# Kernel optimization log

Measured on AMD Instinct MI355X. Metric: run time of the kernel, lower is better.

The kernel has to match this reference:

```python
import jax, jax.numpy as jnp
import numpy as np

N_NODES = 100000
N_EDGES = 1600000
F_IN = 512
HEADS = 8
C1 = 8            # hidden per head in conv1
N_CLASSES = 40
NEG_SLOPE = 0.2
EPS = 1e-16


def setup_inputs() -> dict:
    key = jax.random.key(0)
    ks = jax.random.split(key, 12)
    x = jax.random.normal(ks[0], (N_NODES, F_IN), dtype=jnp.float32)
    # edges with src != dst (PyG SuperGAT removes then re-adds self-loops)
    src = jax.random.randint(ks[1], (N_EDGES,), 0, N_NODES)
    off = jax.random.randint(ks[2], (N_EDGES,), 1, N_NODES)
    dst = (src + off) % N_NODES
    edge_index = jnp.stack([src, dst]).astype(jnp.int64)
    def glorot(k, shape):
        fan = shape[0] + shape[-1]
        return jax.random.uniform(k, shape, jnp.float32, -1.0, 1.0) * np.sqrt(6.0 / fan)
    W1 = glorot(ks[3], (F_IN, HEADS * C1))
    att_l1 = glorot(ks[4], (HEADS, C1))
    att_r1 = glorot(ks[5], (HEADS, C1))
    b1 = jnp.zeros((HEADS * C1,), jnp.float32)
    W2 = glorot(ks[6], (HEADS * C1, HEADS * N_CLASSES))
    att_l2 = glorot(ks[7], (HEADS, N_CLASSES))
    att_r2 = glorot(ks[8], (HEADS, N_CLASSES))
    b2 = jnp.zeros((N_CLASSES,), jnp.float32)
    return {"x": x, "edge_index": edge_index, "W1": W1, "att_l1": att_l1,
            "att_r1": att_r1, "b1": b1, "W2": W2, "att_l2": att_l2,
            "att_r2": att_r2, "b2": b2}


def supergat_conv(x, edge_index, W, att_l, att_r, bias, concat):
    """SuperGATConv with attention_type='MX', eval mode (no dropout)."""
    N = x.shape[0]
    H, C = att_l.shape
    xw = (x @ W).reshape(N, H, C)
    loops = jnp.arange(N)
    src = jnp.concatenate([edge_index[0], loops])  # j (source)
    dst = jnp.concatenate([edge_index[1], loops])  # i (target)
    x_j = xw[src]                                   # [E,H,C]
    x_i = xw[dst]                                   # [E,H,C]
    # MX attention: GO score gated by sigmoid of DP logits
    logits = jnp.einsum('ehc,ehc->eh', x_i, x_j)
    alpha = jnp.einsum('ehc,hc->eh', x_j, att_l) + jnp.einsum('ehc,hc->eh', x_i, att_r)
    alpha = alpha * jax.nn.sigmoid(logits)
    alpha = jax.nn.leaky_relu(alpha, NEG_SLOPE)
    # segment softmax over incoming edges of each destination node
    amax = jax.ops.segment_max(alpha, dst, num_segments=N)
    e = jnp.exp(alpha - amax[dst])
    denom = jax.ops.segment_sum(e, dst, num_segments=N)
    a = e / (denom[dst] + EPS)
    out = jax.ops.segment_sum(x_j * a[..., None], dst, num_segments=N)  # [N,H,C]
    out = out.reshape(N, H * C) if concat else out.mean(axis=1)
    return out + bias


def reference(x, edge_index, W1, att_l1, att_r1, b1, W2, att_l2, att_r2, b2):
    # eval mode: F.dropout(p=0.6) is identity, att_loss is 0
    h = jax.nn.elu(supergat_conv(x, edge_index, W1, att_l1, att_r1, b1, concat=True))
    out = supergat_conv(h, edge_index, W2, att_l2, att_r2, b2, concat=False)
    att_loss = jnp.float32(0.0)
    return jax.nn.log_softmax(out, axis=-1), att_loss
```

## Files before the change

kernel.cpp:

```cpp
#include <hip/hip_runtime.h>
#include <cstdint>

#define N_NODES 100000
#define N_EDGES 1600000
#define SCAN_NB 196

typedef short bf16x8 __attribute__((ext_vector_type(8)));
typedef float f32x4 __attribute__((ext_vector_type(4)));
typedef float f32x2 __attribute__((ext_vector_type(2)));

__device__ __forceinline__ uint16_t f2bf(float f) {
    uint32_t b = __float_as_uint(f);
    return (uint16_t)((b + 0x7fffu + ((b >> 16) & 1u)) >> 16);
}
__device__ __forceinline__ float bfval(uint16_t u) {
    return __uint_as_float(((uint32_t)u) << 16);
}
__device__ __forceinline__ float blo(uint32_t u) { return __uint_as_float(u << 16); }
__device__ __forceinline__ float bhi(uint32_t u) { return __uint_as_float(u & 0xffff0000u); }

__global__ void cvt_w1(const float* __restrict__ W1, uint16_t* __restrict__ whi,
                       uint16_t* __restrict__ wlo) {
    int gid = blockIdx.x * 256 + threadIdx.x;
    int c = gid & 63, kg = gid >> 6;
    uint32_t dh[4], dl[4];
    #pragma unroll
    for (int t = 0; t < 4; ++t) {
        float v0 = W1[(kg * 8 + 2 * t) * 64 + c];
        float v1 = W1[(kg * 8 + 2 * t + 1) * 64 + c];
        uint16_t h0 = f2bf(v0), h1 = f2bf(v1);
        uint16_t l0 = f2bf(v0 - bfval(h0)), l1 = f2bf(v1 - bfval(h1));
        dh[t] = h0 | ((uint32_t)h1 << 16);
        dl[t] = l0 | ((uint32_t)l1 << 16);
    }
    *(uint4*)(whi + (long)c * 512 + kg * 8) = make_uint4(dh[0], dh[1], dh[2], dh[3]);
    *(uint4*)(wlo + (long)c * 512 + kg * 8) = make_uint4(dl[0], dl[1], dl[2], dl[3]);
}

__global__ void cvt_w2(const float* __restrict__ W2, uint16_t* __restrict__ w2T) {
    int c = blockIdx.x * 64 + threadIdx.x;
    if (c >= 320) return;
    for (int kg = 0; kg < 8; ++kg) {
        uint32_t d[4];
        #pragma unroll
        for (int t = 0; t < 4; ++t) {
            float v0 = W2[(kg * 8 + 2 * t) * 320 + c];
            float v1 = W2[(kg * 8 + 2 * t + 1) * 320 + c];
            d[t] = f2bf(v0) | ((uint32_t)f2bf(v1) << 16);
        }
        *(uint4*)(w2T + (long)c * 64 + kg * 8) = make_uint4(d[0], d[1], d[2], d[3]);
    }
}

__global__ __launch_bounds__(256) void wvec_k(const float* __restrict__ W2,
        const float* __restrict__ attl, const float* __restrict__ attr,
        float* __restrict__ wl2, float* __restrict__ wr2) {
    int t = blockIdx.x * 256 + threadIdx.x;
    if (t >= 512) return;
    int h = t >> 6, k = t & 63;
    float sl = 0.f, sr = 0.f;
    #pragma unroll 8
    for (int c = 0; c < 40; ++c) {
        float w = W2[k * 320 + h * 40 + c];
        sl += w * attl[h * 40 + c];
        sr += w * attr[h * 40 + c];
    }
    wl2[t] = sl; wr2[t] = sr;
}

__global__ __launch_bounds__(512) void gemm1_mfma(const float* __restrict__ x,
        const uint16_t* __restrict__ w1hi, const uint16_t* __restrict__ w1lo,
        float* __restrict__ xw1) {
    __shared__ __align__(16) char Ah[128 * 144];
    __shared__ __align__(16) char Al[128 * 144];
    __shared__ __align__(16) char Bh[64 * 144];
    __shared__ __align__(16) char Bl[64 * 144];
    int tid = threadIdx.x;
    int l = tid & 63, w = tid >> 6;
    long base = (long)blockIdx.x * 128;
    f32x4 acc[4];
    #pragma unroll
    for (int ct = 0; ct < 4; ++ct)
        #pragma unroll
        for (int j = 0; j < 4; ++j) acc[ct][j] = 0.f;

    for (int kb = 0; kb < 512; kb += 64) {
        __syncthreads();
        #pragma unroll
        for (int it = 0; it < 2; ++it) {
            int idx = tid + it * 512;
            int row = idx >> 3, kc = idx & 7;
            long r = base + row; if (r >= N_NODES) r = N_NODES - 1;
            const float4* p = (const float4*)(x + r * 512 + kb + kc * 8);
            float4 f0 = p[0], f1 = p[1];
            float v[8] = {f0.x, f0.y, f0.z, f0.w, f1.x, f1.y, f1.z, f1.w};
            uint32_t dh[4], dl[4];
            #pragma unroll
            for (int t = 0; t < 4; ++t) {
                uint16_t h0 = f2bf(v[2 * t]),     h1 = f2bf(v[2 * t + 1]);
                uint16_t l0 = f2bf(v[2 * t] - bfval(h0));
                uint16_t l1 = f2bf(v[2 * t + 1] - bfval(h1));
                dh[t] = h0 | ((uint32_t)h1 << 16);
                dl[t] = l0 | ((uint32_t)l1 << 16);
            }
            *(uint4*)(Ah + row * 144 + kc * 16) = make_uint4(dh[0], dh[1], dh[2], dh[3]);
            *(uint4*)(Al + row * 144 + kc * 16) = make_uint4(dl[0], dl[1], dl[2], dl[3]);
        }
        {
            int c = tid >> 3, kc = tid & 7;
            *(uint4*)(Bh + c * 144 + kc * 16) =
                *(const uint4*)(w1hi + (long)c * 512 + kb + kc * 8);
            *(uint4*)(Bl + c * 144 + kc * 16) =
                *(const uint4*)(w1lo + (long)c * 512 + kb + kc * 8);
        }
        __syncthreads();
        #pragma unroll
        for (int kk = 0; kk < 2; ++kk) {
            int aoff = (w * 16 + (l & 15)) * 144 + kk * 64 + (l >> 4) * 16;
            bf16x8 ah = *(const bf16x8*)(Ah + aoff);
            bf16x8 alo = *(const bf16x8*)(Al + aoff);
            #pragma unroll
            for (int ct = 0; ct < 4; ++ct) {
                int boff = (ct * 16 + (l & 15)) * 144 + kk * 64 + (l >> 4) * 16;
                bf16x8 bh = *(const bf16x8*)(Bh + boff);
                bf16x8 bl = *(const bf16x8*)(Bl + boff);
                acc[ct] = __builtin_amdgcn_mfma_f32_16x16x32_bf16(ah, bh, acc[ct], 0, 0, 0);
                acc[ct] = __builtin_amdgcn_mfma_f32_16x16x32_bf16(alo, bh, acc[ct], 0, 0, 0);
                acc[ct] = __builtin_amdgcn_mfma_f32_16x16x32_bf16(ah, bl, acc[ct], 0, 0, 0);
            }
        }
    }
    int nrow = w * 16 + (l >> 4) * 4;
    #pragma unroll
    for (int ct = 0; ct < 4; ++ct)
        #pragma unroll
        for (int j = 0; j < 4; ++j) {
            long node = base + nrow + j;
            if (node < N_NODES) xw1[node * 64 + ct * 16 + (l & 15)] = acc[ct][j];
        }
}

__global__ __launch_bounds__(512) void gemm2_mfma(const float* __restrict__ h,
        const uint16_t* __restrict__ w2T, uint16_t* __restrict__ xw2) {
    __shared__ __align__(16) char Bsm[320 * 144];
    int tid = threadIdx.x;
    int l = tid & 63, w = tid >> 6;
    long base = (long)blockIdx.x * 128;
    #pragma unroll
    for (int it = 0; it < 5; ++it) {
        int idx = tid + it * 512;
        int c = idx >> 3, kc = idx & 7;
        *(uint4*)(Bsm + c * 144 + kc * 16) = *(const uint4*)(w2T + (long)c * 64 + kc * 8);
    }
    long n0 = base + w * 16 + (l & 15);
    long nld = n0 < N_NODES ? n0 : N_NODES - 1;
    bf16x8 ah[2], alo[2];
    #pragma unroll
    for (int kk = 0; kk < 2; ++kk) {
        const float4* p = (const float4*)(h + nld * 64 + kk * 32 + (l >> 4) * 8);
        float4 f0 = p[0], f1 = p[1];
        float v[8] = {f0.x, f0.y, f0.z, f0.w, f1.x, f1.y, f1.z, f1.w};
        bf16x8 hv, lv;
        #pragma unroll
        for (int t = 0; t < 8; ++t) {
            uint16_t hh = f2bf(v[t]);
            hv[t] = (short)hh;
            lv[t] = (short)f2bf(v[t] - bfval(hh));
        }
        ah[kk] = hv; alo[kk] = lv;
    }
    __syncthreads();
    f32x4 acc[20];
    #pragma unroll
    for (int ct = 0; ct < 20; ++ct)
        #pragma unroll
        for (int j = 0; j < 4; ++j) acc[ct][j] = 0.f;
    #pragma unroll
    for (int ct = 0; ct < 20; ++ct) {
        #pragma unroll
        for (int kk = 0; kk < 2; ++kk) {
            bf16x8 b = *(const bf16x8*)(Bsm + (ct * 16 + (l & 15)) * 144 + kk * 64 + (l >> 4) * 16);
            acc[ct] = __builtin_amdgcn_mfma_f32_16x16x32_bf16(b, ah[kk], acc[ct], 0, 0, 0);
            acc[ct] = __builtin_amdgcn_mfma_f32_16x16x32_bf16(b, alo[kk], acc[ct], 0, 0, 0);
        }
    }
    if (n0 < N_NODES) {
        #pragma unroll
        for (int ct = 0; ct < 20; ++ct) {
            uint32_t d0 = f2bf(acc[ct][0]) | ((uint32_t)f2bf(acc[ct][1]) << 16);
            uint32_t d1 = f2bf(acc[ct][2]) | ((uint32_t)f2bf(acc[ct][3]) << 16);
            int cb = ct * 16 + (l >> 4) * 4;
            *(uint32_t*)(xw2 + n0 * 320 + cb) = d0;
            *(uint32_t*)(xw2 + n0 * 320 + cb + 2) = d1;
        }
    }
}

__global__ void hist_k(const int* __restrict__ dst, int* __restrict__ deg) {
    int e = blockIdx.x * blockDim.x + threadIdx.x;
    if (e < N_EDGES) atomicAdd(&deg[dst[e]], 1);
}

__global__ __launch_bounds__(512) void scan_a(const int* __restrict__ deg,
        int* __restrict__ offs, int* __restrict__ btot) {
    __shared__ int sh[512];
    int t = threadIdx.x;
    int g = blockIdx.x * 512 + t;
    int v = (g < N_NODES) ? deg[g] : 0;
    sh[t] = v;
    __syncthreads();
    #pragma unroll
    for (int o = 1; o < 512; o <<= 1) {
        int add = (t >= o) ? sh[t - o] : 0;
        __syncthreads();
        sh[t] += add;
        __syncthreads();
    }
    if (g < N_NODES) offs[g] = sh[t] - v;
    if (t == 511) btot[blockIdx.x] = sh[511];
}

__global__ __launch_bounds__(256) void scan_b(int* __restrict__ btot) {
    __shared__ int sh[256];
    int t = threadIdx.x;
    int v = (t < SCAN_NB) ? btot[t] : 0;
    sh[t] = v;
    __syncthreads();
    #pragma unroll
    for (int o = 1; o < 256; o <<= 1) {
        int add = (t >= o) ? sh[t - o] : 0;
        __syncthreads();
        sh[t] += add;
        __syncthreads();
    }
    if (t < SCAN_NB) btot[t] = sh[t] - v;
}

__global__ __launch_bounds__(512) void scan_c(int* __restrict__ offs,
        const int* __restrict__ btot, int* __restrict__ cursor) {
    int g = blockIdx.x * 512 + threadIdx.x;
    if (g < N_NODES) {
        int o = offs[g] + btot[blockIdx.x];
        offs[g] = o;
        cursor[g] = o;
    }
}

__global__ void scatter_k(const int* __restrict__ src, const int* __restrict__ dst,
        int* __restrict__ cursor, int* __restrict__ csr8) {
    int e = blockIdx.x * blockDim.x + threadIdx.x;
    if (e < N_EDGES) {
        int pos = atomicAdd(&cursor[dst[e]], 1);
        csr8[pos] = src[e] << 3;
    }
}

__global__ __launch_bounds__(256) void conv1_node(const float* __restrict__ xw,
        const int* __restrict__ offs, const int* __restrict__ deg,
        const int* __restrict__ csr8, const float* __restrict__ att_l,
        const float* __restrict__ att_r, const float* __restrict__ b1,
        float* __restrict__ hout) {
    int wid = (blockIdx.x * blockDim.x + threadIdx.x) >> 6;
    if (wid >= N_NODES) return;
    int i = wid;
    int lane = threadIdx.x & 63;
    int g = lane >> 3, h = lane & 7;
    const float4* rowi = (const float4*)(xw + (long)i * 64 + h * 8);
    float4 xi0 = rowi[0], xi1 = rowi[1];
    f32x2 xip[4] = {{xi0.x, xi0.y}, {xi0.z, xi0.w}, {xi1.x, xi1.y}, {xi1.z, xi1.w}};
    const float4* alp4 = (const float4*)(att_l + h * 8);
    float4 t0 = alp4[0], t1 = alp4[1];
    f32x2 atlp[4] = {{t0.x, t0.y}, {t0.z, t0.w}, {t1.x, t1.y}, {t1.z, t1.w}};
    const float4* arp4 = (const float4*)(att_r + h * 8);
    float4 u0 = arp4[0], u1 = arp4[1];
    f32x2 atrp[4] = {{u0.x, u0.y}, {u0.z, u0.w}, {u1.x, u1.y}, {u1.z, u1.w}};
    f32x2 prp = xip[0] * atrp[0];
    prp += xip[1] * atrp[1];
    prp += xip[2] * atrp[2];
    prp += xip[3] * atrp[3];
    float pr = prp.x + prp.y;
    f32x2 accp[4] = {{0.f,0.f},{0.f,0.f},{0.f,0.f},{0.f,0.f}};
    float den = 0.f;

#define C1_EDGE(XJP) do { \
    f32x2 qdp = xip[0] * (XJP)[0]; \
    qdp += xip[1] * (XJP)[1]; \
    qdp += xip[2] * (XJP)[2]; \
    qdp += xip[3] * (XJP)[3]; \
    f32x2 qlp = (XJP)[0] * atlp[0]; \
    qlp += (XJP)[1] * atlp[1]; \
    qlp += (XJP)[2] * atlp[2]; \
    qlp += (XJP)[3] * atlp[3]; \
    float qd = qdp.x + qdp.y, ql = qlp.x + qlp.y; \
    float a = (ql + pr) / (1.0f + __expf(-qd)); \
    a = a > 0.f ? a : 0.2f * a; \
    float e = __expf(a); \
    den += e; \
    f32x2 ev = {e, e}; \
    accp[0] += ev * (XJP)[0]; \
    accp[1] += ev * (XJP)[1]; \
    accp[2] += ev * (XJP)[2]; \
    accp[3] += ev * (XJP)[3]; \
} while (0)

    if (g == 0) C1_EDGE(xip);
    int off = offs[i], dg = deg[i];
    int k = g;
    for (; k + 8 < dg; k += 16) {
        int j0 = csr8[off + k], j1 = csr8[off + k + 8];
        const float4* r0 = (const float4*)(xw + (long)j0 * 8 + h * 8);
        const float4* r1 = (const float4*)(xw + (long)j1 * 8 + h * 8);
        float4 a0 = r0[0], a1 = r0[1];
        float4 b0 = r1[0], b1v = r1[1];
        f32x2 ap[4] = {{a0.x, a0.y}, {a0.z, a0.w}, {a1.x, a1.y}, {a1.z, a1.w}};
        f32x2 bp[4] = {{b0.x, b0.y}, {b0.z, b0.w}, {b1v.x, b1v.y}, {b1v.z, b1v.w}};
        C1_EDGE(ap);
        C1_EDGE(bp);
    }
    if (k < dg) {
        int j0 = csr8[off + k];
        const float4* r0 = (const float4*)(xw + (long)j0 * 8 + h * 8);
        float4 a0 = r0[0], a1 = r0[1];
        f32x2 ap[4] = {{a0.x, a0.y}, {a0.z, a0.w}, {a1.x, a1.y}, {a1.z, a1.w}};
        C1_EDGE(ap);
    }
#undef C1_EDGE

    float acc[8] = {accp[0].x, accp[0].y, accp[1].x, accp[1].y,
                    accp[2].x, accp[2].y, accp[3].x, accp[3].y};
    #pragma unroll
    for (int o = 8; o <= 32; o <<= 1) {
        #pragma unroll
        for (int t = 0; t < 8; ++t) acc[t] += __shfl_xor(acc[t], o);
        den += __shfl_xor(den, o);
    }
    if (g == 0) {
        float inv = 1.0f / (den + 1e-16f);
        const float4* bp4 = (const float4*)(b1 + h * 8);
        float4 c0 = bp4[0], c1 = bp4[1];
        float4 o0, o1;
        float v;
        v = acc[0]*inv + c0.x; o0.x = v > 0.f ? v : __expf(v) - 1.0f;
        v = acc[1]*inv + c0.y; o0.y = v > 0.f ? v : __expf(v) - 1.0f;
        v = acc[2]*inv + c0.z; o0.z = v > 0.f ? v : __expf(v) - 1.0f;
        v = acc[3]*inv + c0.w; o0.w = v > 0.f ? v : __expf(v) - 1.0f;
        v = acc[4]*inv + c1.x; o1.x = v > 0.f ? v : __expf(v) - 1.0f;
        v = acc[5]*inv + c1.y; o1.y = v > 0.f ? v : __expf(v) - 1.0f;
        v = acc[6]*inv + c1.z; o1.z = v > 0.f ? v : __expf(v) - 1.0f;
        v = acc[7]*inv + c1.w; o1.w = v > 0.f ? v : __expf(v) - 1.0f;
        float4* po = (float4*)(hout + (long)i * 64 + h * 8);
        po[0] = o0; po[1] = o1;
    }
}

__global__ __launch_bounds__(256) void node_att2h(const float* __restrict__ hbuf,
        const float* __restrict__ wl2, const float* __restrict__ wr2,
        float* __restrict__ al, float* __restrict__ ar) {
    __shared__ float lw[512], lr[512];
    int tid = threadIdx.x;
    for (int t = tid; t < 512; t += 256) { lw[t] = wl2[t]; lr[t] = wr2[t]; }
    __syncthreads();
    int i = blockIdx.x * 256 + tid;
    if (i >= N_NODES) return;
    const float4* row = (const float4*)(hbuf + (long)i * 64);
    float sl[8] = {0,0,0,0,0,0,0,0}, sr[8] = {0,0,0,0,0,0,0,0};
    #pragma unroll
    for (int d4 = 0; d4 < 16; ++d4) {
        float4 v = row[d4];
        #pragma unroll
        for (int hh = 0; hh < 8; ++hh) {
            const float4 wv = *(const float4*)(lw + hh * 64 + d4 * 4);
            const float4 rv = *(const float4*)(lr + hh * 64 + d4 * 4);
            sl[hh] += v.x*wv.x + v.y*wv.y + v.z*wv.z + v.w*wv.w;
            sr[hh] += v.x*rv.x + v.y*rv.y + v.z*rv.z + v.w*rv.w;
        }
    }
    #pragma unroll
    for (int hh = 0; hh < 8; ++hh) {
        al[i * 8 + hh] = sl[hh];
        ar[i * 8 + hh] = sr[hh];
    }
}

__global__ __launch_bounds__(256) void conv2_node(const uint16_t* __restrict__ xw,
        const int* __restrict__ offs, const int* __restrict__ deg,
        const int* __restrict__ csr8, const float* __restrict__ al,
        const float* __restrict__ ar, const float* __restrict__ b2,
        float* __restrict__ out) {
    if (blockIdx.x == 0 && threadIdx.x == 0) out[(long)N_NODES * 40] = 0.0f;
    int wid = (blockIdx.x * blockDim.x + threadIdx.x) >> 6;
    if (wid >= N_NODES) return;
    int i = wid;
    int lane = threadIdx.x & 63;
    int half = lane >> 5, l = lane & 31;
    int h = l >> 2;
    const uint32_t* xwd = (const uint32_t*)xw;
    const uint32_t* rowi = xwd + (long)i * 160 + 5 * l;
    f32x2 xip[5];
    #pragma unroll
    for (int t = 0; t < 5; ++t) { uint32_t u = rowi[t]; xip[t] = (f32x2){blo(u), bhi(u)}; }
    float ari = ar[i * 8 + h];
    f32x2 accp[5] = {{0.f,0.f},{0.f,0.f},{0.f,0.f},{0.f,0.f},{0.f,0.f}};
    float den = 0.f;

#define LOADP(DST, SRC) do { \
    _Pragma("unroll") \
    for (int t = 0; t < 5; ++t) { uint32_t u = (SRC)[t]; (DST)[t] = (f32x2){blo(u), bhi(u)}; } \
} while (0)

#define C2_BODY(ALJ, XJP) do { \
    f32x2 pdp = xip[0] * (XJP)[0]; \
    pdp += xip[1] * (XJP)[1]; \
    pdp += xip[2] * (XJP)[2]; \
    pdp += xip[3] * (XJP)[3]; \
    pdp += xip[4] * (XJP)[4]; \
    float pd = pdp.x + pdp.y; \
    pd += __shfl_xor(pd, 1); \
    pd += __shfl_xor(pd, 2); \
    float a = (ALJ) + ari; \
    a = a / (1.0f + __expf(-pd)); \
    a = a > 0.f ? a : 0.2f * a; \
    float e = __expf(a); \
    den += e; \
    f32x2 ev = {e, e}; \
    accp[0] += ev * (XJP)[0]; \
    accp[1] += ev * (XJP)[1]; \
    accp[2] += ev * (XJP)[2]; \
    accp[3] += ev * (XJP)[3]; \
    accp[4] += ev * (XJP)[4]; \
} while (0)

    if (half == 0) C2_BODY(al[i * 8 + h], xip);
    int off = offs[i], dg = deg[i];
    int k = half;
    for (; k + 2 < dg; k += 4) {
        int j0 = csr8[off + k], j1 = csr8[off + k + 2];
        const uint32_t* r0 = xwd + (long)j0 * 20 + 5 * l;
        const uint32_t* r1 = xwd + (long)j1 * 20 + 5 * l;
        f32x2 a0p[5], a1p[5];
        LOADP(a0p, r0);
        LOADP(a1p, r1);
        float e0 = al[j0 + h], e1 = al[j1 + h];
        C2_BODY(e0, a0p);
        C2_BODY(e1, a1p);
    }
    if (k < dg) {
        int j0 = csr8[off + k];
        const uint32_t* r0 = xwd + (long)j0 * 20 + 5 * l;
        f32x2 a0p[5];
        LOADP(a0p, r0);
        float e0 = al[j0 + h];
        C2_BODY(e0, a0p);
    }
#undef C2_BODY
#undef LOADP

    float acc[10] = {accp[0].x, accp[0].y, accp[1].x, accp[1].y, accp[2].x,
                     accp[2].y, accp[3].x, accp[3].y, accp[4].x, accp[4].y};
    #pragma unroll
    for (int t = 0; t < 10; ++t) acc[t] += __shfl_xor(acc[t], 32);
    den += __shfl_xor(den, 32);
    float inv = 0.125f / (den + 1e-16f);
    #pragma unroll
    for (int t = 0; t < 10; ++t) acc[t] *= inv;
    #pragma unroll
    for (int o = 4; o <= 16; o <<= 1) {
        #pragma unroll
        for (int t = 0; t < 10; ++t) acc[t] += __shfl_xor(acc[t], o);
    }
    int q = lane & 3;
    #pragma unroll
    for (int t = 0; t < 10; ++t) acc[t] += b2[10 * q + t];
    float mx = acc[0];
    #pragma unroll
    for (int t = 1; t < 10; ++t) mx = fmaxf(mx, acc[t]);
    mx = fmaxf(mx, __shfl_xor(mx, 1));
    mx = fmaxf(mx, __shfl_xor(mx, 2));
    float s = 0.f;
    #pragma unroll
    for (int t = 0; t < 10; ++t) s += __expf(acc[t] - mx);
    s += __shfl_xor(s, 1);
    s += __shfl_xor(s, 2);
    float lse = mx + logf(s);
    if (lane < 4) {
        float2* po = (float2*)(out + (long)i * 40 + 10 * q);
        #pragma unroll
        for (int t = 0; t < 5; ++t)
            po[t] = make_float2(acc[2 * t] - lse, acc[2 * t + 1] - lse);
    }
}

extern "C" void kernel_launch(void* const* d_in, const int* in_sizes, int n_in,
                              void* d_out, int out_size, void* d_ws, size_t ws_size,
                              hipStream_t stream) {
    const float* x      = (const float*)d_in[0];
    const int*   ei     = (const int*)d_in[1];
    const float* W1     = (const float*)d_in[2];
    const float* att_l1 = (const float*)d_in[3];
    const float* att_r1 = (const float*)d_in[4];
    const float* b1     = (const float*)d_in[5];
    const float* W2     = (const float*)d_in[6];
    const float* att_l2 = (const float*)d_in[7];
    const float* att_r2 = (const float*)d_in[8];
    const float* b2     = (const float*)d_in[9];
    const int* src = ei;
    const int* dst = ei + N_EDGES;
    float* out = (float*)d_out;

    char* ws = (char*)d_ws;
    float*    xw1    = (float*)(ws + 0);
    float*    hbuf   = (float*)(ws + 25600000);
    uint16_t* xw2b   = (uint16_t*)(ws + 51200000);
    float*    al     = (float*)(ws + 115200000);
    float*    ar     = (float*)(ws + 118400000);
    int*      deg    = (int*)(ws + 121600000);
    int*      offs   = (int*)(ws + 122000000);
    int*      cursor = (int*)(ws + 122400000);
    int*      btot   = (int*)(ws + 122800000);
    int*      csr8   = (int*)(ws + 122801024);
    uint16_t* w1hi   = (uint16_t*)(ws + 129201024);
    uint16_t* w1lo   = (uint16_t*)(ws + 129266560);
    uint16_t* w2T    = (uint16_t*)(ws + 129332096);
    float*    wl2    = (float*)(ws + 129373056);
    float*    wr2    = (float*)(ws + 129375104);

    hipMemsetAsync(deg, 0, (size_t)N_NODES * 4, stream);

    cvt_w1<<<16, 256, 0, stream>>>(W1, w1hi, w1lo);
    cvt_w2<<<5, 64, 0, stream>>>(W2, w2T);
    wvec_k<<<2, 256, 0, stream>>>(W2, att_l2, att_r2, wl2, wr2);

    hist_k<<<6250, 256, 0, stream>>>(dst, deg);
    scan_a<<<SCAN_NB, 512, 0, stream>>>(deg, offs, btot);
    scan_b<<<1, 256, 0, stream>>>(btot);
    scan_c<<<SCAN_NB, 512, 0, stream>>>(offs, btot, cursor);
    scatter_k<<<6250, 256, 0, stream>>>(src, dst, cursor, csr8);

    gemm1_mfma<<<782, 512, 0, stream>>>(x, w1hi, w1lo, xw1);
    conv1_node<<<25000, 256, 0, stream>>>(xw1, offs, deg, csr8, att_l1, att_r1, b1, hbuf);
    node_att2h<<<391, 256, 0, stream>>>(hbuf, wl2, wr2, al, ar);

    gemm2_mfma<<<782, 512, 0, stream>>>(hbuf, w2T, xw2b);
    conv2_node<<<25000, 256, 0, stream>>>(xw2b, offs, deg, csr8, al, ar, b2, out);
}
```

Before: 539.1 us.

## Software-pipeline conv2 neighbor gathers and use fast rcp, DPP reductions, vector loads

Restructures the conv2 edge loop into a double-buffered software pipeline that prefetches the next pair of neighbor rows (and their attention logits) while computing the current pair, hiding gather latency. Changes the per-lane column layout so each lane loads a uint4 plus one word instead of five scalar words, with matching bias and output layout (float4 stores). Replaces divisions with hardware reciprocal approximations, intra-quad shuffles with DPP adds, and logf with __logf in both conv kernels. Adds register pressure and slightly lower numerical precision.

```diff
diff --git a/kernel.cpp b/kernel.cpp
--- a/kernel.cpp
+++ b/kernel.cpp
@@ -18,6 +18,16 @@
 }
 __device__ __forceinline__ float blo(uint32_t u) { return __uint_as_float(u << 16); }
 __device__ __forceinline__ float bhi(uint32_t u) { return __uint_as_float(u & 0xffff0000u); }
+
+__device__ __forceinline__ float fast_rcp(float x) { return __builtin_amdgcn_rcpf(x); }
+__device__ __forceinline__ float dpp_xadd1(float x) {
+    int s = __builtin_amdgcn_update_dpp(0, __float_as_int(x), 0xB1, 0xF, 0xF, true);
+    return x + __int_as_float(s);
+}
+__device__ __forceinline__ float dpp_xadd2(float x) {
+    int s = __builtin_amdgcn_update_dpp(0, __float_as_int(x), 0x4E, 0xF, 0xF, true);
+    return x + __int_as_float(s);
+}
 
 __global__ void cvt_w1(const float* __restrict__ W1, uint16_t* __restrict__ whi,
                        uint16_t* __restrict__ wlo) {
@@ -292,8 +302,8 @@
     qlp += (XJP)[2] * atlp[2]; \
     qlp += (XJP)[3] * atlp[3]; \
     float qd = qdp.x + qdp.y, ql = qlp.x + qlp.y; \
-    float a = (ql + pr) / (1.0f + __expf(-qd)); \
-    a = a > 0.f ? a : 0.2f * a; \
+    float a = (ql + pr) * fast_rcp(1.0f + __expf(-qd)); \
+    a = fmaxf(a, 0.2f * a); \
     float e = __expf(a); \
     den += e; \
     f32x2 ev = {e, e}; \
@@ -335,7 +345,7 @@
         den += __shfl_xor(den, o);
     }
     if (g == 0) {
-        float inv = 1.0f / (den + 1e-16f);
+        float inv = fast_rcp(den + 1e-16f);
         const float4* bp4 = (const float4*)(b1 + h * 8);
         float4 c0 = bp4[0], c1 = bp4[1];
         float4 o0, o1;
@@ -382,6 +392,12 @@
     }
 }
 
+__device__ __forceinline__ int fidx(const int* __restrict__ csr8, int pos, int valid) {
+    int p = pos < N_EDGES ? pos : N_EDGES - 1;
+    int j = csr8[p];
+    return valid ? j : 0;
+}
+
 __global__ __launch_bounds__(256) void conv2_node(const uint16_t* __restrict__ xw,
         const int* __restrict__ offs, const int* __restrict__ deg,
         const int* __restrict__ csr8, const float* __restrict__ al,
@@ -393,33 +409,37 @@
     int i = wid;
     int lane = threadIdx.x & 63;
     int half = lane >> 5, l = lane & 31;
-    int h = l >> 2;
+    int h = l >> 2, q = l & 3;
     const uint32_t* xwd = (const uint32_t*)xw;
-    const uint32_t* rowi = xwd + (long)i * 160 + 5 * l;
+    unsigned lq4 = 20u * (unsigned)h + 4u * (unsigned)q;
+    unsigned lq1 = 20u * (unsigned)h + 16u + (unsigned)q;
+
     f32x2 xip[5];
-    #pragma unroll
-    for (int t = 0; t < 5; ++t) { uint32_t u = rowi[t]; xip[t] = (f32x2){blo(u), bhi(u)}; }
+    {
+        const uint32_t* rowi = xwd + (unsigned)i * 160u;
+        uint4 qi = *(const uint4*)(rowi + lq4);
+        uint32_t ti = rowi[lq1];
+        xip[0] = (f32x2){blo(qi.x), bhi(qi.x)};
+        xip[1] = (f32x2){blo(qi.y), bhi(qi.y)};
+        xip[2] = (f32x2){blo(qi.z), bhi(qi.z)};
+        xip[3] = (f32x2){blo(qi.w), bhi(qi.w)};
+        xip[4] = (f32x2){blo(ti),   bhi(ti)};
+    }
     float ari = ar[i * 8 + h];
     f32x2 accp[5] = {{0.f,0.f},{0.f,0.f},{0.f,0.f},{0.f,0.f},{0.f,0.f}};
     float den = 0.f;
 
-#define LOADP(DST, SRC) do { \
-    _Pragma("unroll") \
-    for (int t = 0; t < 5; ++t) { uint32_t u = (SRC)[t]; (DST)[t] = (f32x2){blo(u), bhi(u)}; } \
-} while (0)
-
-#define C2_BODY(ALJ, XJP) do { \
+#define C2_CORE(ALJ, XJP) do { \
     f32x2 pdp = xip[0] * (XJP)[0]; \
     pdp += xip[1] * (XJP)[1]; \
     pdp += xip[2] * (XJP)[2]; \
     pdp += xip[3] * (XJP)[3]; \
     pdp += xip[4] * (XJP)[4]; \
     float pd = pdp.x + pdp.y; \
-    pd += __shfl_xor(pd, 1); \
-    pd += __shfl_xor(pd, 2); \
-    float a = (ALJ) + ari; \
-    a = a / (1.0f + __expf(-pd)); \
-    a = a > 0.f ? a : 0.2f * a; \
+    pd = dpp_xadd1(pd); \
+    pd = dpp_xadd2(pd); \
+    float a = ((ALJ) + ari) * fast_rcp(1.0f + __expf(-pd)); \
+    a = fmaxf(a, 0.2f * a); \
     float e = __expf(a); \
     den += e; \
     f32x2 ev = {e, e}; \
@@ -430,37 +450,60 @@
     accp[4] += ev * (XJP)[4]; \
 } while (0)
 
-    if (half == 0) C2_BODY(al[i * 8 + h], xip);
+#define C2_UNPACK(DST, U) do { \
+    _Pragma("unroll") \
+    for (int t = 0; t < 5; ++t) (DST)[t] = (f32x2){blo((U)[t]), bhi((U)[t])}; \
+} while (0)
+
+#define C2_FETCH(J, BUF, ALV) do { \
+    const uint32_t* _r = xwd + (unsigned)(J) * 20u; \
+    uint4 _q = *(const uint4*)(_r + lq4); \
+    (BUF)[0] = _q.x; (BUF)[1] = _q.y; (BUF)[2] = _q.z; (BUF)[3] = _q.w; \
+    (BUF)[4] = _r[lq1]; \
+    (ALV) = al[(J) + h]; \
+} while (0)
+
+    if (half == 0) C2_CORE(al[i * 8 + h], xip);
     int off = offs[i], dg = deg[i];
+
     int k = half;
-    for (; k + 2 < dg; k += 4) {
-        int j0 = csr8[off + k], j1 = csr8[off + k + 2];
-        const uint32_t* r0 = xwd + (long)j0 * 20 + 5 * l;
-        const uint32_t* r1 = xwd + (long)j1 * 20 + 5 * l;
-        f32x2 a0p[5], a1p[5];
-        LOADP(a0p, r0);
-        LOADP(a1p, r1);
-        float e0 = al[j0 + h], e1 = al[j1 + h];
-        C2_BODY(e0, a0p);
-        C2_BODY(e1, a1p);
-    }
-    if (k < dg) {
-        int j0 = csr8[off + k];
-        const uint32_t* r0 = xwd + (long)j0 * 20 + 5 * l;
-        f32x2 a0p[5];
-        LOADP(a0p, r0);
-        float e0 = al[j0 + h];
-        C2_BODY(e0, a0p);
-    }
-#undef C2_BODY
-#undef LOADP
+    int v0 = (k < dg), v1 = (k + 2 < dg);
+    int j0 = fidx(csr8, off + k, v0);
+    int j1 = fidx(csr8, off + k + 2, v1);
+    uint32_t cA[5], cB[5], dA[5], dB[5];
+    float alA, alB, alC, alD;
+    C2_FETCH(j0, cA, alA);
+    C2_FETCH(j1, cB, alB);
+    while (v0) {
+        int k4 = k + 4;
+        int w0 = (k4 < dg), w1 = (k4 + 2 < dg);
+        int m0 = fidx(csr8, off + k4, w0);
+        int m1 = fidx(csr8, off + k4 + 2, w1);
+        C2_FETCH(m0, dA, alC);
+        C2_FETCH(m1, dB, alD);
+        { f32x2 xj[5]; C2_UNPACK(xj, cA); C2_CORE(alA, xj); }
+        if (v1) { f32x2 xj[5]; C2_UNPACK(xj, cB); C2_CORE(alB, xj); }
+        if (!w0) break;
+        int k8 = k + 8;
+        v0 = (k8 < dg); v1 = (k8 + 2 < dg);
+        int p0 = fidx(csr8, off + k8, v0);
+        int p1 = fidx(csr8, off + k8 + 2, v1);
+        C2_FETCH(p0, cA, alA);
+        C2_FETCH(p1, cB, alB);
+        { f32x2 xj[5]; C2_UNPACK(xj, dA); C2_CORE(alC, xj); }
+        if (w1) { f32x2 xj[5]; C2_UNPACK(xj, dB); C2_CORE(alD, xj); }
+        k = k8;
+    }
+#undef C2_CORE
+#undef C2_UNPACK
+#undef C2_FETCH
 
     float acc[10] = {accp[0].x, accp[0].y, accp[1].x, accp[1].y, accp[2].x,
                      accp[2].y, accp[3].x, accp[3].y, accp[4].x, accp[4].y};
     #pragma unroll
     for (int t = 0; t < 10; ++t) acc[t] += __shfl_xor(acc[t], 32);
     den += __shfl_xor(den, 32);
-    float inv = 0.125f / (den + 1e-16f);
+    float inv = 0.125f * fast_rcp(den + 1e-16f);
     #pragma unroll
     for (int t = 0; t < 10; ++t) acc[t] *= inv;
     #pragma unroll
@@ -468,9 +511,10 @@
         #pragma unroll
         for (int t = 0; t < 10; ++t) acc[t] += __shfl_xor(acc[t], o);
     }
-    int q = lane & 3;
-    #pragma unroll
-    for (int t = 0; t < 10; ++t) acc[t] += b2[10 * q + t];
+    #pragma unroll
+    for (int t = 0; t < 8; ++t) acc[t] += b2[8 * q + t];
+    acc[8] += b2[32 + 2 * q];
+    acc[9] += b2[33 + 2 * q];
     float mx = acc[0];
     #pragma unroll
     for (int t = 1; t < 10; ++t) mx = fmaxf(mx, acc[t]);
@@ -481,12 +525,13 @@
     for (int t = 0; t < 10; ++t) s += __expf(acc[t] - mx);
     s += __shfl_xor(s, 1);
     s += __shfl_xor(s, 2);
-    float lse = mx + logf(s);
+    float lse = mx + __logf(s);
     if (lane < 4) {
-        float2* po = (float2*)(out + (long)i * 40 + 10 * q);
-        #pragma unroll
-        for (int t = 0; t < 5; ++t)
-            po[t] = make_float2(acc[2 * t] - lse, acc[2 * t + 1] - lse);
+        float4* po = (float4*)(out + (long)i * 40 + 8 * q);
+        po[0] = make_float4(acc[0] - lse, acc[1] - lse, acc[2] - lse, acc[3] - lse);
+        po[1] = make_float4(acc[4] - lse, acc[5] - lse, acc[6] - lse, acc[7] - lse);
+        float2* pt = (float2*)(out + (long)i * 40 + 32 + 2 * q);
+        *pt = make_float2(acc[8] - lse, acc[9] - lse);
     }
 }
 
```

Measured after the change: 538.0 us. About the same (-0.2%).

## Restructure conv2 to gather 64-dim hidden features via precomputed W2 Gram products

Applied to the files above, without the earlier changes.

Layer 2 used to gather 320-wide projected rows per edge. It now gathers the 64-wide bf16 hidden rows and computes the dot-product logits as h_j·(M_h h_i), where M_h = W2_h W2_h^T is precomputed and Y = M h_i comes from a new per-node GEMM. Aggregation runs in the 64-dim space, and W2 is applied once per node from LDS after normalization. This cuts per-edge gather bandwidth about fivefold. The costs are a larger per-node Y tensor, 40 KB of LDS per block, extra shuffles, and bf16 rounding of the hidden features. Division is also replaced with a hardware reciprocal approximation.

```diff
diff --git a/kernel.cpp b/kernel.cpp
--- a/kernel.cpp
+++ b/kernel.cpp
@@ -18,6 +18,8 @@
 }
 __device__ __forceinline__ float blo(uint32_t u) { return __uint_as_float(u << 16); }
 __device__ __forceinline__ float bhi(uint32_t u) { return __uint_as_float(u & 0xffff0000u); }
+
+__device__ __forceinline__ float fast_rcp(float x) { return __builtin_amdgcn_rcpf(x); }
 
 __global__ void cvt_w1(const float* __restrict__ W1, uint16_t* __restrict__ whi,
                        uint16_t* __restrict__ wlo) {
@@ -35,21 +37,6 @@
     }
     *(uint4*)(whi + (long)c * 512 + kg * 8) = make_uint4(dh[0], dh[1], dh[2], dh[3]);
     *(uint4*)(wlo + (long)c * 512 + kg * 8) = make_uint4(dl[0], dl[1], dl[2], dl[3]);
-}
-
-__global__ void cvt_w2(const float* __restrict__ W2, uint16_t* __restrict__ w2T) {
-    int c = blockIdx.x * 64 + threadIdx.x;
-    if (c >= 320) return;
-    for (int kg = 0; kg < 8; ++kg) {
-        uint32_t d[4];
-        #pragma unroll
-        for (int t = 0; t < 4; ++t) {
-            float v0 = W2[(kg * 8 + 2 * t) * 320 + c];
-            float v1 = W2[(kg * 8 + 2 * t + 1) * 320 + c];
-            d[t] = f2bf(v0) | ((uint32_t)f2bf(v1) << 16);
-        }
-        *(uint4*)(w2T + (long)c * 64 + kg * 8) = make_uint4(d[0], d[1], d[2], d[3]);
-    }
 }
 
 __global__ __launch_bounds__(256) void wvec_k(const float* __restrict__ W2,
@@ -66,6 +53,41 @@
         sr += w * attr[h * 40 + c];
     }
     wl2[t] = sl; wr2[t] = sr;
+}
+
+__global__ __launch_bounds__(512) void mcat_k(const float* __restrict__ W2,
+        uint16_t* __restrict__ mhi, uint16_t* __restrict__ mlo) {
+    __shared__ float Wh[64 * 40];
+    int h = blockIdx.x;
+    int tid = threadIdx.x;
+    for (int t = tid; t < 2560; t += 512) {
+        int k = t / 40, c = t % 40;
+        Wh[k * 40 + c] = W2[k * 320 + h * 40 + c];
+    }
+    __syncthreads();
+    #pragma unroll
+    for (int r = 0; r < 8; ++r) {
+        int o = r * 512 + tid;
+        int kp = o >> 6, k = o & 63;
+        float s = 0.f;
+        #pragma unroll 8
+        for (int c = 0; c < 40; ++c) s += Wh[k * 40 + c] * Wh[kp * 40 + c];
+        uint16_t hi = f2bf(s);
+        uint16_t lo = f2bf(s - bfval(hi));
+        mhi[(h * 64 + kp) * 64 + k] = hi;
+        mlo[(h * 64 + kp) * 64 + k] = lo;
+    }
+}
+
+__global__ __launch_bounds__(256) void w2l_k(const float* __restrict__ W2,
+        uint16_t* __restrict__ w2lg) {
+    int t = blockIdx.x * 256 + threadIdx.x;
+    if (t >= 20480) return;
+    int s = t & 3, tmp = t >> 2;
+    int cc = tmp % 10; tmp /= 10;
+    int G = tmp & 3; tmp >>= 2;
+    int h = tmp & 7; int g = tmp >> 3;
+    w2lg[t] = f2bf(W2[(4 * g + s) * 320 + h * 40 + 10 * G + cc]);
 }
 
 __global__ __launch_bounds__(512) void gemm1_mfma(const float* __restrict__ x,
@@ -140,58 +162,56 @@
         }
 }
 
-__global__ __launch_bounds__(512) void gemm2_mfma(const float* __restrict__ h,
-        const uint16_t* __restrict__ w2T, uint16_t* __restrict__ xw2) {
-    __shared__ __align__(16) char Bsm[320 * 144];
+__global__ __launch_bounds__(512) void ygemm_mfma(const uint16_t* __restrict__ hjb,
+        const uint16_t* __restrict__ mhi, const uint16_t* __restrict__ mlo,
+        uint16_t* __restrict__ Y16) {
+    __shared__ __align__(16) char Bh[256 * 144];
+    __shared__ __align__(16) char Bl[256 * 144];
     int tid = threadIdx.x;
     int l = tid & 63, w = tid >> 6;
-    long base = (long)blockIdx.x * 128;
-    #pragma unroll
-    for (int it = 0; it < 5; ++it) {
+    int half = blockIdx.x & 1;
+    long base = (long)(blockIdx.x >> 1) * 128;
+    #pragma unroll
+    for (int it = 0; it < 4; ++it) {
         int idx = tid + it * 512;
         int c = idx >> 3, kc = idx & 7;
-        *(uint4*)(Bsm + c * 144 + kc * 16) = *(const uint4*)(w2T + (long)c * 64 + kc * 8);
+        *(uint4*)(Bh + c * 144 + kc * 16) =
+            *(const uint4*)(mhi + (long)(half * 256 + c) * 64 + kc * 8);
+        *(uint4*)(Bl + c * 144 + kc * 16) =
+            *(const uint4*)(mlo + (long)(half * 256 + c) * 64 + kc * 8);
     }
     long n0 = base + w * 16 + (l & 15);
     long nld = n0 < N_NODES ? n0 : N_NODES - 1;
-    bf16x8 ah[2], alo[2];
-    #pragma unroll
-    for (int kk = 0; kk < 2; ++kk) {
-        const float4* p = (const float4*)(h + nld * 64 + kk * 32 + (l >> 4) * 8);
-        float4 f0 = p[0], f1 = p[1];
-        float v[8] = {f0.x, f0.y, f0.z, f0.w, f1.x, f1.y, f1.z, f1.w};
-        bf16x8 hv, lv;
-        #pragma unroll
-        for (int t = 0; t < 8; ++t) {
-            uint16_t hh = f2bf(v[t]);
-            hv[t] = (short)hh;
-            lv[t] = (short)f2bf(v[t] - bfval(hh));
-        }
-        ah[kk] = hv; alo[kk] = lv;
-    }
+    bf16x8 a[2];
+    #pragma unroll
+    for (int kk = 0; kk < 2; ++kk)
+        a[kk] = *(const bf16x8*)(hjb + nld * 64 + kk * 32 + (l >> 4) * 8);
     __syncthreads();
-    f32x4 acc[20];
-    #pragma unroll
-    for (int ct = 0; ct < 20; ++ct)
+    f32x4 acc[16];
+    #pragma unroll
+    for (int ct = 0; ct < 16; ++ct)
         #pragma unroll
         for (int j = 0; j < 4; ++j) acc[ct][j] = 0.f;
     #pragma unroll
-    for (int ct = 0; ct < 20; ++ct) {
+    for (int ct = 0; ct < 16; ++ct) {
         #pragma unroll
         for (int kk = 0; kk < 2; ++kk) {
-            bf16x8 b = *(const bf16x8*)(Bsm + (ct * 16 + (l & 15)) * 144 + kk * 64 + (l >> 4) * 16);
-            acc[ct] = __builtin_amdgcn_mfma_f32_16x16x32_bf16(b, ah[kk], acc[ct], 0, 0, 0);
-            acc[ct] = __builtin_amdgcn_mfma_f32_16x16x32_bf16(b, alo[kk], acc[ct], 0, 0, 0);
+            bf16x8 bh = *(const bf16x8*)(Bh + (ct * 16 + (l & 15)) * 144 + kk * 64 + (l >> 4) * 16);
+            bf16x8 bl = *(const bf16x8*)(Bl + (ct * 16 + (l & 15)) * 144 + kk * 64 + (l >> 4) * 16);
+            acc[ct] = __builtin_amdgcn_mfma_f32_16x16x32_bf16(bh, a[kk], acc[ct], 0, 0, 0);
+            acc[ct] = __builtin_amdgcn_mfma_f32_16x16x32_bf16(bl, a[kk], acc[ct], 0, 0, 0);
         }
     }
     if (n0 < N_NODES) {
-        #pragma unroll
-        for (int ct = 0; ct < 20; ++ct) {
+        uint32_t* Yd = (uint32_t*)Y16;
+        #pragma unroll
+        for (int ct = 0; ct < 16; ++ct) {
+            int kp = half * 256 + ct * 16 + (l >> 4) * 4;
+            int k2 = kp & 63, hh = kp >> 6, gg = k2 >> 2;
             uint32_t d0 = f2bf(acc[ct][0]) | ((uint32_t)f2bf(acc[ct][1]) << 16);
             uint32_t d1 = f2bf(acc[ct][2]) | ((uint32_t)f2bf(acc[ct][3]) << 16);
-            int cb = ct * 16 + (l >> 4) * 4;
-            *(uint32_t*)(xw2 + n0 * 320 + cb) = d0;
-            *(uint32_t*)(xw2 + n0 * 320 + cb + 2) = d1;
+            Yd[n0 * 256 + gg * 16 + hh * 2]     = d0;
+            Yd[n0 * 256 + gg * 16 + hh * 2 + 1] = d1;
         }
     }
 }
@@ -259,7 +279,7 @@
         const int* __restrict__ offs, const int* __restrict__ deg,
         const int* __restrict__ csr8, const float* __restrict__ att_l,
         const float* __restrict__ att_r, const float* __restrict__ b1,
-        float* __restrict__ hout) {
+        float* __restrict__ hout, uint16_t* __restrict__ hjb) {
     int wid = (blockIdx.x * blockDim.x + threadIdx.x) >> 6;
     if (wid >= N_NODES) return;
     int i = wid;
@@ -292,8 +312,8 @@
     qlp += (XJP)[2] * atlp[2]; \
     qlp += (XJP)[3] * atlp[3]; \
     float qd = qdp.x + qdp.y, ql = qlp.x + qlp.y; \
-    float a = (ql + pr) / (1.0f + __expf(-qd)); \
-    a = a > 0.f ? a : 0.2f * a; \
+    float a = (ql + pr) * fast_rcp(1.0f + __expf(-qd)); \
+    a = fmaxf(a, 0.2f * a); \
     float e = __expf(a); \
     den += e; \
     f32x2 ev = {e, e}; \
@@ -335,7 +355,7 @@
         den += __shfl_xor(den, o);
     }
     if (g == 0) {
-        float inv = 1.0f / (den + 1e-16f);
+        float inv = fast_rcp(den + 1e-16f);
         const float4* bp4 = (const float4*)(b1 + h * 8);
         float4 c0 = bp4[0], c1 = bp4[1];
         float4 o0, o1;
@@ -350,6 +370,11 @@
         v = acc[7]*inv + c1.w; o1.w = v > 0.f ? v : __expf(v) - 1.0f;
         float4* po = (float4*)(hout + (long)i * 64 + h * 8);
         po[0] = o0; po[1] = o1;
+        uint32_t d0 = f2bf(o0.x) | ((uint32_t)f2bf(o0.y) << 16);
+        uint32_t d1 = f2bf(o0.z) | ((uint32_t)f2bf(o0.w) << 16);
+        uint32_t d2 = f2bf(o1.x) | ((uint32_t)f2bf(o1.y) << 16);
+        uint32_t d3 = f2bf(o1.z) | ((uint32_t)f2bf(o1.w) << 16);
+        *(uint4*)(hjb + (long)i * 64 + h * 8) = make_uint4(d0, d1, d2, d3);
     }
 }
 
@@ -382,111 +407,181 @@
     }
 }
 
-__global__ __launch_bounds__(256) void conv2_node(const uint16_t* __restrict__ xw,
+__global__ __launch_bounds__(256) void conv2_node(const uint16_t* __restrict__ hjb16,
         const int* __restrict__ offs, const int* __restrict__ deg,
         const int* __restrict__ csr8, const float* __restrict__ al,
-        const float* __restrict__ ar, const float* __restrict__ b2,
+        const float* __restrict__ ar, const uint16_t* __restrict__ Y16,
+        const uint16_t* __restrict__ w2lg, const float* __restrict__ b2,
         float* __restrict__ out) {
+    __shared__ __align__(16) uint16_t W2L[20480];
+    for (int t = threadIdx.x; t < 2560; t += 256)
+        ((uint4*)W2L)[t] = ((const uint4*)w2lg)[t];
+    __syncthreads();
     if (blockIdx.x == 0 && threadIdx.x == 0) out[(long)N_NODES * 40] = 0.0f;
-    int wid = (blockIdx.x * blockDim.x + threadIdx.x) >> 6;
+    int wid = (blockIdx.x * 256 + threadIdx.x) >> 6;
     if (wid >= N_NODES) return;
     int i = wid;
     int lane = threadIdx.x & 63;
-    int half = lane >> 5, l = lane & 31;
-    int h = l >> 2;
-    const uint32_t* xwd = (const uint32_t*)xw;
-    const uint32_t* rowi = xwd + (long)i * 160 + 5 * l;
-    f32x2 xip[5];
-    #pragma unroll
-    for (int t = 0; t < 5; ++t) { uint32_t u = rowi[t]; xip[t] = (f32x2){blo(u), bhi(u)}; }
-    float ari = ar[i * 8 + h];
-    f32x2 accp[5] = {{0.f,0.f},{0.f,0.f},{0.f,0.f},{0.f,0.f},{0.f,0.f}};
+    int g = lane & 15, G = lane >> 4, lam = lane & 7;
+    const uint32_t* hjd = (const uint32_t*)hjb16;
+    const uint32_t* Yd  = (const uint32_t*)Y16;
+
+    f32x2 y[8][2];
+    #pragma unroll
+    for (int m = 0; m < 8; ++m) {
+        uint2 d = *(const uint2*)(Yd + (size_t)i * 256 + g * 16 + ((lam ^ m) * 2));
+        y[m][0] = (f32x2){blo(d.x), bhi(d.x)};
+        y[m][1] = (f32x2){blo(d.y), bhi(d.y)};
+    }
+    float ari = ar[i * 8 + lam];
+    float b2v[10];
+    #pragma unroll
+    for (int cc = 0; cc < 10; ++cc) b2v[cc] = b2[10 * G + cc];
+
+    f32x2 agg[8][2];
+    #pragma unroll
+    for (int m = 0; m < 8; ++m) { agg[m][0] = (f32x2){0.f,0.f}; agg[m][1] = (f32x2){0.f,0.f}; }
     float den = 0.f;
-
-#define LOADP(DST, SRC) do { \
-    _Pragma("unroll") \
-    for (int t = 0; t < 5; ++t) { uint32_t u = (SRC)[t]; (DST)[t] = (f32x2){blo(u), bhi(u)}; } \
-} while (0)
-
-#define C2_BODY(ALJ, XJP) do { \
-    f32x2 pdp = xip[0] * (XJP)[0]; \
-    pdp += xip[1] * (XJP)[1]; \
-    pdp += xip[2] * (XJP)[2]; \
-    pdp += xip[3] * (XJP)[3]; \
-    pdp += xip[4] * (XJP)[4]; \
-    float pd = pdp.x + pdp.y; \
-    pd += __shfl_xor(pd, 1); \
-    pd += __shfl_xor(pd, 2); \
-    float a = (ALJ) + ari; \
-    a = a / (1.0f + __expf(-pd)); \
-    a = a > 0.f ? a : 0.2f * a; \
-    float e = __expf(a); \
-    den += e; \
-    f32x2 ev = {e, e}; \
-    accp[0] += ev * (XJP)[0]; \
-    accp[1] += ev * (XJP)[1]; \
-    accp[2] += ev * (XJP)[2]; \
-    accp[3] += ev * (XJP)[3]; \
-    accp[4] += ev * (XJP)[4]; \
-} while (0)
-
-    if (half == 0) C2_BODY(al[i * 8 + h], xip);
     int off = offs[i], dg = deg[i];
-    int k = half;
-    for (; k + 2 < dg; k += 4) {
-        int j0 = csr8[off + k], j1 = csr8[off + k + 2];
-        const uint32_t* r0 = xwd + (long)j0 * 20 + 5 * l;
-        const uint32_t* r1 = xwd + (long)j1 * 20 + 5 * l;
-        f32x2 a0p[5], a1p[5];
-        LOADP(a0p, r0);
-        LOADP(a1p, r1);
-        float e0 = al[j0 + h], e1 = al[j1 + h];
-        C2_BODY(e0, a0p);
-        C2_BODY(e1, a1p);
-    }
-    if (k < dg) {
-        int j0 = csr8[off + k];
-        const uint32_t* r0 = xwd + (long)j0 * 20 + 5 * l;
-        f32x2 a0p[5];
-        LOADP(a0p, r0);
-        float e0 = al[j0 + h];
-        C2_BODY(e0, a0p);
-    }
-#undef C2_BODY
-#undef LOADP
-
-    float acc[10] = {accp[0].x, accp[0].y, accp[1].x, accp[1].y, accp[2].x,
-                     accp[2].y, accp[3].x, accp[3].y, accp[4].x, accp[4].y};
-    #pragma unroll
-    for (int t = 0; t < 10; ++t) acc[t] += __shfl_xor(acc[t], 32);
+
+    auto CORE = [&](uint2 d, float alv, bool valid) {
+        f32x2 h0 = {blo(d.x), bhi(d.x)}, h1 = {blo(d.y), bhi(d.y)};
+        float pd[8];
+        #pragma unroll
+        for (int m = 0; m < 8; ++m) {
+            f32x2 t = y[m][0] * h0;
+            t += y[m][1] * h1;
+            pd[m] = t.x + t.y;
+        }
+        #pragma unroll
+        for (int m = 0; m < 4; ++m) pd[m] += __shfl_xor(pd[m + 4], 4);
+        pd[0] += __shfl_xor(pd[2], 2);
+        pd[1] += __shfl_xor(pd[3], 2);
+        pd[0] += __shfl_xor(pd[1], 1);
+        pd[0] += __shfl_xor(pd[0], 8);
+        float a = (alv + ari) * fast_rcp(1.0f + __expf(-pd[0]));
+        a = fmaxf(a, 0.2f * a);
+        float e = __expf(a);
+        e = valid ? e : 0.f;
+        den += e;
+        float f0 = e;
+        float f[8]; f[0] = f0;
+        #pragma unroll
+        for (int m = 1; m < 8; ++m) f[m] = __shfl_xor(f0, m);
+        #pragma unroll
+        for (int m = 0; m < 8; ++m) {
+            f32x2 ev = {f[m], f[m]};
+            agg[m][0] += ev * h0;
+            agg[m][1] += ev * h1;
+        }
+    };
+
+    {
+        uint2 ds = *(const uint2*)(hjd + (size_t)i * 32 + g * 2);
+        float als = al[i * 8 + lam];
+        CORE(ds, als, G == 0);
+    }
+
+    auto IDX = [&](int S) -> int {
+        int e = G + 4 * S;
+        int p = off + e;
+        p = p < N_EDGES ? p : 0;
+        int j = csr8[p];
+        return e < dg ? j : 0;
+    };
+    auto FETCH = [&](int j, uint2& d, float& a2) {
+        d = *(const uint2*)(hjd + (size_t)j * 4 + g * 2);
+        a2 = al[j + lam];
+    };
+
+    int nT = (dg + 3) >> 2;
+    uint2 D0, D1; float A0v, A1v;
+    {
+        int j0 = IDX(0); FETCH(j0, D0, A0v);
+        int j1 = IDX(1); FETCH(j1, D1, A1v);
+    }
+    int s = 0;
+    while (s + 2 <= nT) {
+        int j2 = IDX(s + 2);
+        CORE(D0, A0v, G + 4 * s < dg);
+        FETCH(j2, D0, A0v);
+        int j3 = IDX(s + 3);
+        CORE(D1, A1v, G + 4 * (s + 1) < dg);
+        FETCH(j3, D1, A1v);
+        s += 2;
+    }
+    if (s < nT)     CORE(D0, A0v, G + 4 * s < dg);
+    if (s + 1 < nT) CORE(D1, A1v, G + 4 * (s + 1) < dg);
+
+    #pragma unroll
+    for (int m = 0; m < 8; ++m) {
+        #pragma unroll
+        for (int p = 0; p < 2; ++p) {
+            f32x2 t16 = {__shfl_xor(agg[m][p].x, 16), __shfl_xor(agg[m][p].y, 16)};
+            agg[m][p] += t16;
+            f32x2 t32 = {__shfl_xor(agg[m][p].x, 32), __shfl_xor(agg[m][p].y, 32)};
+            agg[m][p] += t32;
+        }
+    }
+    den += __shfl_xor(den, 16);
     den += __shfl_xor(den, 32);
-    float inv = 0.125f / (den + 1e-16f);
-    #pragma unroll
-    for (int t = 0; t < 10; ++t) acc[t] *= inv;
-    #pragma unroll
-    for (int o = 4; o <= 16; o <<= 1) {
-        #pragma unroll
-        for (int t = 0; t < 10; ++t) acc[t] += __shfl_xor(acc[t], o);
-    }
-    int q = lane & 3;
-    #pragma unroll
-    for (int t = 0; t < 10; ++t) acc[t] += b2[10 * q + t];
-    float mx = acc[0];
-    #pragma unroll
-    for (int t = 1; t < 10; ++t) mx = fmaxf(mx, acc[t]);
-    mx = fmaxf(mx, __shfl_xor(mx, 1));
-    mx = fmaxf(mx, __shfl_xor(mx, 2));
-    float s = 0.f;
-    #pragma unroll
-    for (int t = 0; t < 10; ++t) s += __expf(acc[t] - mx);
-    s += __shfl_xor(s, 1);
-    s += __shfl_xor(s, 2);
-    float lse = mx + logf(s);
-    if (lane < 4) {
-        float2* po = (float2*)(out + (long)i * 40 + 10 * q);
+    #pragma unroll
+    for (int m = 0; m < 8; ++m) {
+        float dm = (m == 0) ? den : __shfl_xor(den, m);
+        float inv = 0.125f * fast_rcp(dm + 1e-16f);
+        f32x2 iv = {inv, inv};
+        agg[m][0] *= iv;
+        agg[m][1] *= iv;
+    }
+
+    f32x2 o2[10];
+    #pragma unroll
+    for (int cc = 0; cc < 10; ++cc) o2[cc] = (f32x2){0.f, 0.f};
+    #pragma unroll
+    for (int m = 0; m < 8; ++m) {
+        const uint16_t* wp = W2L + (((g * 8 + (lam ^ m)) * 4 + G) * 40);
+        uint4 wq0 = *(const uint4*)(wp);
+        uint4 wq1 = *(const uint4*)(wp + 8);
+        uint4 wq2 = *(const uint4*)(wp + 16);
+        uint4 wq3 = *(const uint4*)(wp + 24);
+        uint4 wq4 = *(const uint4*)(wp + 32);
+        uint32_t wdw[20] = {wq0.x, wq0.y, wq0.z, wq0.w, wq1.x, wq1.y, wq1.z, wq1.w,
+                            wq2.x, wq2.y, wq2.z, wq2.w, wq3.x, wq3.y, wq3.z, wq3.w,
+                            wq4.x, wq4.y, wq4.z, wq4.w};
+        #pragma unroll
+        for (int cc = 0; cc < 10; ++cc) {
+            f32x2 w0p = {blo(wdw[2 * cc]), bhi(wdw[2 * cc])};
+            f32x2 w1p = {blo(wdw[2 * cc + 1]), bhi(wdw[2 * cc + 1])};
+            o2[cc] += agg[m][0] * w0p;
+            o2[cc] += agg[m][1] * w1p;
+        }
+    }
+    float o[10];
+    #pragma unroll
+    for (int cc = 0; cc < 10; ++cc) o[cc] = o2[cc].x + o2[cc].y;
+    #pragma unroll
+    for (int r = 1; r <= 8; r <<= 1) {
+        #pragma unroll
+        for (int cc = 0; cc < 10; ++cc) o[cc] += __shfl_xor(o[cc], r);
+    }
+    #pragma unroll
+    for (int cc = 0; cc < 10; ++cc) o[cc] += b2v[cc];
+    float mx = o[0];
+    #pragma unroll
+    for (int cc = 1; cc < 10; ++cc) mx = fmaxf(mx, o[cc]);
+    mx = fmaxf(mx, __shfl_xor(mx, 16));
+    mx = fmaxf(mx, __shfl_xor(mx, 32));
+    float sm = 0.f;
+    #pragma unroll
+    for (int cc = 0; cc < 10; ++cc) sm += __expf(o[cc] - mx);
+    sm += __shfl_xor(sm, 16);
+    sm += __shfl_xor(sm, 32);
+    float lse = mx + __logf(sm);
+    if (g == 0) {
+        float2* po = (float2*)(out + (long)i * 40 + 10 * G);
         #pragma unroll
         for (int t = 0; t < 5; ++t)
-            po[t] = make_float2(acc[2 * t] - lse, acc[2 * t + 1] - lse);
+            po[t] = make_float2(o[2 * t] - lse, o[2 * t + 1] - lse);
     }
 }
 
@@ -508,9 +603,10 @@
     float* out = (float*)d_out;
 
     char* ws = (char*)d_ws;
+    uint16_t* Y      = (uint16_t*)(ws + 0);
     float*    xw1    = (float*)(ws + 0);
     float*    hbuf   = (float*)(ws + 25600000);
-    uint16_t* xw2b   = (uint16_t*)(ws + 51200000);
+    uint16_t* hjb    = (uint16_t*)(ws + 102400000);
     float*    al     = (float*)(ws + 115200000);
     float*    ar     = (float*)(ws + 118400000);
     int*      deg    = (int*)(ws + 121600000);
@@ -520,15 +616,18 @@
     int*      csr8   = (int*)(ws + 122801024);
     uint16_t* w1hi   = (uint16_t*)(ws + 129201024);
     uint16_t* w1lo   = (uint16_t*)(ws + 129266560);
-    uint16_t* w2T    = (uint16_t*)(ws + 129332096);
-    float*    wl2    = (float*)(ws + 129373056);
-    float*    wr2    = (float*)(ws + 129375104);
+    uint16_t* mhi    = (uint16_t*)(ws + 129332096);
+    uint16_t* mlo    = (uint16_t*)(ws + 129397632);
+    uint16_t* w2lg   = (uint16_t*)(ws + 129463168);
+    float*    wl2    = (float*)(ws + 129504128);
+    float*    wr2    = (float*)(ws + 129506176);
 
     hipMemsetAsync(deg, 0, (size_t)N_NODES * 4, stream);
 
     cvt_w1<<<16, 256, 0, stream>>>(W1, w1hi, w1lo);
-    cvt_w2<<<5, 64, 0, stream>>>(W2, w2T);
     wvec_k<<<2, 256, 0, stream>>>(W2, att_l2, att_r2, wl2, wr2);
+    mcat_k<<<8, 512, 0, stream>>>(W2, mhi, mlo);
+    w2l_k<<<80, 256, 0, stream>>>(W2, w2lg);
 
     hist_k<<<6250, 256, 0, stream>>>(dst, deg);
     scan_a<<<SCAN_NB, 512, 0, stream>>>(deg, offs, btot);
@@ -537,9 +636,11 @@
     scatter_k<<<6250, 256, 0, stream>>>(src, dst, cursor, csr8);
 
     gemm1_mfma<<<782, 512, 0, stream>>>(x, w1hi, w1lo, xw1);
-    conv1_node<<<25000, 256, 0, stream>>>(xw1, offs, deg, csr8, att_l1, att_r1, b1, hbuf);
+    conv1_node<<<25000, 256, 0, stream>>>(xw1, offs, deg, csr8, att_l1, att_r1, b1,
+                                          hbuf, hjb);
     node_att2h<<<391, 256, 0, stream>>>(hbuf, wl2, wr2, al, ar);
 
-    gemm2_mfma<<<782, 512, 0, stream>>>(hbuf, w2T, xw2b);
-    conv2_node<<<25000, 256, 0, stream>>>(xw2b, offs, deg, csr8, al, ar, b2, out);
-}
+    ygemm_mfma<<<1564, 512, 0, stream>>>(hjb, mhi, mlo, Y);
+
+    conv2_node<<<25000, 256, 0, stream>>>(hjb, offs, deg, csr8, al, ar, Y, w2lg, b2, out);
+}
```

Result: slower. 828.9 us (+53.8%).
